# Kernel optimization log

Measured on AMD Instinct MI355X. Metric: run time of the kernel, lower is better.

## Reference

```python
import math
import jax, jax.numpy as jnp
import numpy as np

B, DIM, L = 2, 512, 2048
H = 16
HD = DIM // H  # 32
R = 32
K = 3
GAMMA = 1.0


def _conv1d(x, w, b=None):
    # x: [B, Cin, L], w: [Cout, Cin, K] -> [B, Cout, L_out] (VALID)
    out = jax.lax.conv_general_dilated(
        x, w, window_strides=(1,), padding='VALID',
        dimension_numbers=('NCH', 'OIH', 'NCH'))
    if b is not None:
        out = out + b[None, :, None]
    return out


def _sketch_p4(x, G1, G2):
    # x: [B, H, L, HD]; G1, G2: [HD, R]
    # p=4: half = (1/sqrt(r)) * (x@G1 * x@G2); return half*half
    half = (x @ G1) * (x @ G2) / math.sqrt(R)
    return half * half  # [B, H, L, R]


def setup_inputs() -> dict:
    key = jax.random.key(0)
    ks = jax.random.split(key, 12)
    x = jax.random.normal(ks[0], (B, DIM, L), dtype=jnp.float32)
    # conv / linear params (kaiming-ish scale)
    q_w = jax.random.normal(ks[1], (DIM, DIM, K), dtype=jnp.float32) / math.sqrt(DIM * K)
    q_b = jnp.zeros((DIM,), dtype=jnp.float32)
    k_w = jax.random.normal(ks[2], (DIM, DIM, K), dtype=jnp.float32) / math.sqrt(DIM * K)
    k_b = jnp.zeros((DIM,), dtype=jnp.float32)
    v_w = jax.random.normal(ks[3], (DIM, DIM, 1), dtype=jnp.float32) / math.sqrt(DIM)
    proj_w = jax.random.normal(ks[4], (DIM, DIM), dtype=jnp.float32) / math.sqrt(DIM)
    proj_b = jnp.zeros((DIM,), dtype=jnp.float32)
    # learnable scalars
    gamma_q = jnp.ones((1,), dtype=jnp.float32) * GAMMA
    beta_q = jnp.zeros((1,), dtype=jnp.float32)
    gamma_k = jnp.ones((1,), dtype=jnp.float32) * GAMMA
    beta_k = jnp.zeros((1,), dtype=jnp.float32)
    # sketch matrices, std = 1/sqrt(r)
    G1q = jax.random.normal(ks[5], (HD, R), dtype=jnp.float32) / math.sqrt(R)
    G2q = jax.random.normal(ks[6], (HD, R), dtype=jnp.float32) / math.sqrt(R)
    G1k = jax.random.normal(ks[7], (HD, R), dtype=jnp.float32) / math.sqrt(R)
    G2k = jax.random.normal(ks[8], (HD, R), dtype=jnp.float32) / math.sqrt(R)
    return dict(x=x, q_w=q_w, q_b=q_b, k_w=k_w, k_b=k_b, v_w=v_w,
                proj_w=proj_w, proj_b=proj_b,
                gamma_q=gamma_q, beta_q=beta_q, gamma_k=gamma_k, beta_k=beta_k,
                G1q=G1q, G2q=G2q, G1k=G1k, G2k=G2k)


def reference(x, q_w, q_b, k_w, k_b, v_w, proj_w, proj_b,
              gamma_q, beta_q, gamma_k, beta_k, G1q, G2q, G1k, G2k):
    batch, dim, length = x.shape
    # causal left pad by K-1
    x_pad = jnp.pad(x, ((0, 0), (0, 0), (K - 1, 0)))
    q = _conv1d(x_pad, q_w, q_b)   # [B, DIM, L]
    k = _conv1d(x_pad, k_w, k_b)   # [B, DIM, L]
    v = _conv1d(x, v_w)            # [B, DIM, L] (1x1 conv, no bias)

    def shape(t):
        # [B, DIM, L] -> [B, H, HD, L] -> [B, H, L, HD]
        return t.reshape(batch, H, HD, length).transpose(0, 1, 3, 2)

    q, k, v = shape(q), shape(k), shape(v)
    q = gamma_q * q + beta_q
    k = gamma_k * k + beta_k
    phi_q = _sketch_p4(q, G1q, G2q)  # [B, H, L, R]
    phi_k = _sketch_p4(k, G1k, G2k)  # [B, H, L, R]
    scores = jnp.einsum('bhlr,bhmr->bhlm', phi_q, phi_k)  # [B, H, L, L]
    attn = scores / (scores.sum(axis=-1, keepdims=True) + 1e-6)
    o = jnp.einsum('bhlm,bhmd->bhld', attn, v)  # [B, H, L, HD]
    # [B, H, L, HD] -> [B, H, HD, L] -> [B, DIM, L] -> [B, L, DIM]
    o = o.transpose(0, 1, 3, 2).reshape(batch, dim, length).transpose(0, 2, 1)
    return o @ proj_w.T + proj_b
```

## Files before the change

### kernel.cpp

```cpp
#include <hip/hip_runtime.h>
#include <hip/hip_bf16.h>

#define DIMC 512
#define LEN  2048
#define NH   16
#define HD   32
#define RR   32

typedef __bf16 bf8_t __attribute__((ext_vector_type(8)));
typedef float  f4_t  __attribute__((ext_vector_type(4)));

__device__ __forceinline__ void gload16(const void* g, void* l) {
    __builtin_amdgcn_global_load_lds(
        (const __attribute__((address_space(1))) unsigned int*)g,
        (__attribute__((address_space(3))) unsigned int*)l, 16, 0, 0);
}

__global__ __launch_bounds__(256) void prep_kernel(
    const float* __restrict__ x,
    const float* __restrict__ qw, const float* __restrict__ kw,
    const float* __restrict__ vw, const float* __restrict__ pw,
    const float* __restrict__ G1q, const float* __restrict__ G2q,
    const float* __restrict__ G1k, const float* __restrict__ G2k,
    __bf16* __restrict__ xTh, __bf16* __restrict__ xTl,
    __bf16* __restrict__ Wrh, __bf16* __restrict__ Wrl,
    __bf16* __restrict__ pwh, __bf16* __restrict__ pwl,
    __bf16* __restrict__ GTh, __bf16* __restrict__ GTl,
    float* __restrict__ Skv)
{
    const int bid = blockIdx.x;
    const int tid = threadIdx.x;
    if (bid < 512) {
        __shared__ float tile[64][65];
        const int lblk = bid & 31, cblk = (bid >> 5) & 7, b = bid >> 8;
        const int l0 = lblk * 64, c0 = cblk * 64;
        #pragma unroll
        for (int it = 0; it < 4; ++it) {
            int cl = (tid >> 4) + it * 16;
            int ll = (tid & 15) * 4;
            float4 v4 = *reinterpret_cast<const float4*>(
                x + ((size_t)b * DIMC + c0 + cl) * LEN + l0 + ll);
            tile[cl][ll+0] = v4.x; tile[cl][ll+1] = v4.y;
            tile[cl][ll+2] = v4.z; tile[cl][ll+3] = v4.w;
        }
        __syncthreads();
        const int l  = tid & 63;
        const int cs = (tid >> 6) * 16;
        size_t rowbase = ((size_t)b * 2050 + l0 + l + 2) * DIMC + c0;
        #pragma unroll
        for (int half = 0; half < 2; ++half) {
            int c = cs + half * 8;
            bf8_t hi, lo;
            #pragma unroll
            for (int e = 0; e < 8; ++e) {
                float f = tile[c + e][l];
                __bf16 h = (__bf16)f;
                hi[e] = h;
                lo[e] = (__bf16)(f - (float)h);
            }
            *reinterpret_cast<bf8_t*>(xTh + rowbase + c) = hi;
            *reinterpret_cast<bf8_t*>(xTl + rowbase + c) = lo;
        }
        if (lblk == 0 && cblk == 0) {
            size_t pb = (size_t)b * 2050 * DIMC;
            #pragma unroll
            for (int e = 0; e < 4; ++e) {
                int p = tid * 4 + e;
                xTh[pb + p] = (__bf16)0.f;
                xTl[pb + p] = (__bf16)0.f;
            }
        }
    } else if (bid < 9728) {
        int idx = (bid - 512) * 256 + tid;
        int m   = idx / 1536;
        int rem = idx - m * 1536;
        int kk  = rem >> 9;
        int ci  = rem & 511;
        float f;
        if (m < 512)       f = qw[((size_t)m * 512 + ci) * 3 + kk];
        else if (m < 1024) f = kw[((size_t)(m - 512) * 512 + ci) * 3 + kk];
        else               f = (kk == 2) ? vw[(size_t)(m - 1024) * 512 + ci] : 0.f;
        __bf16 h = (__bf16)f;
        Wrh[idx] = h;
        Wrl[idx] = (__bf16)(f - (float)h);
    } else if (bid < 10752) {
        int idx = (bid - 9728) * 256 + tid;
        float f = pw[idx];
        __bf16 h = (__bf16)f;
        pwh[idx] = h;
        pwl[idx] = (__bf16)(f - (float)h);
    } else if (bid < 10884) {
        int idx = (bid - 10752) * 256 + tid;
        if (idx < 33792) Skv[idx] = 0.f;
    } else {
        #pragma unroll
        for (int m = 0; m < 4; ++m) {
            const float* g = (m == 0) ? G1q : (m == 1) ? G2q : (m == 2) ? G1k : G2k;
            #pragma unroll
            for (int e = 0; e < 4; ++e) {
                int i = tid * 4 + e;
                int r = i >> 5, d = i & 31;
                float f = g[d * 32 + r];
                __bf16 h = (__bf16)f;
                GTh[m * 1024 + i] = h;
                GTl[m * 1024 + i] = (__bf16)(f - (float)h);
            }
        }
    }
}

__global__ __launch_bounds__(256) void conv_mfma_kernel(
    const __bf16* __restrict__ xTh, const __bf16* __restrict__ xTl,
    const __bf16* __restrict__ Wrh, const __bf16* __restrict__ Wrl,
    const float* __restrict__ q_b, const float* __restrict__ k_b,
    float* __restrict__ q, float* __restrict__ k, float* __restrict__ v)
{
    __shared__ __bf16 sAh[128 * 32], sAl[128 * 32], sBh[64 * 32], sBl[64 * 32];
    const int b   = blockIdx.z;
    const int mg  = blockIdx.y * 128;
    const int n0  = blockIdx.x * 64;
    const int tid = threadIdx.x;
    const int wave = tid >> 6, lane = tid & 63;
    const int wm = wave >> 1, wn = wave & 1;
    const int lr = lane & 15, k8 = lane >> 4;
    const int sec = mg >> 9;
    const int kks = (sec == 2) ? 2 : 0;

    const __bf16* xh = xTh + (size_t)b * 2050 * DIMC;
    const __bf16* xl = xTl + (size_t)b * 2050 * DIMC;

    f4_t acc[4][2];
    #pragma unroll
    for (int i = 0; i < 4; ++i)
        #pragma unroll
        for (int j = 0; j < 2; ++j)
            #pragma unroll
            for (int e = 0; e < 4; ++e) acc[i][j][e] = 0.f;

    const int sr0 = tid >> 2;
    const int ss  = tid & 3;
    const int sk0 = ((ss ^ ((sr0 >> 1) & 3)) << 3);
    const int sr1 = sr0 + 64;
    const int sk1 = ((ss ^ ((sr1 >> 1) & 3)) << 3);

    for (int kk = kks; kk < 3; ++kk) {
        const __bf16* wAh = Wrh + (size_t)mg * 1536 + kk * 512;
        const __bf16* wAl = Wrl + (size_t)mg * 1536 + kk * 512;
        const __bf16* xbh = xh + (size_t)(n0 + kk) * DIMC;
        const __bf16* xbl = xl + (size_t)(n0 + kk) * DIMC;
        for (int k0 = 0; k0 < 512; k0 += 32) {
            gload16(wAh + (size_t)sr0 * 1536 + k0 + sk0, (char*)sAh + tid * 16);
            gload16(wAh + (size_t)sr1 * 1536 + k0 + sk1, (char*)sAh + (256 + tid) * 16);
            gload16(wAl + (size_t)sr0 * 1536 + k0 + sk0, (char*)sAl + tid * 16);
            gload16(wAl + (size_t)sr1 * 1536 + k0 + sk1, (char*)sAl + (256 + tid) * 16);
            gload16(xbh + (size_t)sr0 * DIMC + k0 + sk0, (char*)sBh + tid * 16);
            gload16(xbl + (size_t)sr0 * DIMC + k0 + sk0, (char*)sBl + tid * 16);
            __syncthreads();
            bf8_t ah[4], al[4], bh[2], bl[2];
            #pragma unroll
            for (int i = 0; i < 4; ++i) {
                int row = wm * 64 + i * 16 + lr;
                int off = row * 64 + ((k8 ^ ((row >> 1) & 3)) << 4);
                ah[i] = *(const bf8_t*)((const char*)sAh + off);
                al[i] = *(const bf8_t*)((const char*)sAl + off);
            }
            #pragma unroll
            for (int j = 0; j < 2; ++j) {
                int row = wn * 32 + j * 16 + lr;
                int off = row * 64 + ((k8 ^ ((row >> 1) & 3)) << 4);
                bh[j] = *(const bf8_t*)((const char*)sBh + off);
                bl[j] = *(const bf8_t*)((const char*)sBl + off);
            }
            #pragma unroll
            for (int i = 0; i < 4; ++i)
                #pragma unroll
                for (int j = 0; j < 2; ++j) {
                    acc[i][j] = __builtin_amdgcn_mfma_f32_16x16x32_bf16(ah[i], bh[j], acc[i][j], 0, 0, 0);
                    acc[i][j] = __builtin_amdgcn_mfma_f32_16x16x32_bf16(ah[i], bl[j], acc[i][j], 0, 0, 0);
                    acc[i][j] = __builtin_amdgcn_mfma_f32_16x16x32_bf16(al[i], bh[j], acc[i][j], 0, 0, 0);
                }
            __syncthreads();
        }
    }
    float* outp = (sec == 0) ? q : (sec == 1) ? k : v;
    const float* bp = (sec == 0) ? q_b : (sec == 1) ? k_b : nullptr;
    const int cob = mg & 511;
    #pragma unroll
    for (int i = 0; i < 4; ++i)
        #pragma unroll
        for (int r = 0; r < 4; ++r) {
            int co = cob + wm * 64 + i * 16 + k8 * 4 + r;
            float bv = bp ? bp[co] : 0.f;
            float* orow = outp + ((size_t)b * DIMC + co) * LEN;
            #pragma unroll
            for (int j = 0; j < 2; ++j)
                orow[n0 + wn * 32 + j * 16 + lr] = acc[i][j][r];
            if (bp) {
                #pragma unroll
                for (int j = 0; j < 2; ++j)
                    orow[n0 + wn * 32 + j * 16 + lr] = acc[i][j][r] + bv;
            }
        }
}

__global__ __launch_bounds__(256) void sketch_mfma_kernel(
    const float* __restrict__ q, const float* __restrict__ k,
    const float* __restrict__ gamma_q, const float* __restrict__ beta_q,
    const float* __restrict__ gamma_k, const float* __restrict__ beta_k,
    const __bf16* __restrict__ GTh, const __bf16* __restrict__ GTl,
    float* __restrict__ phi_q, float* __restrict__ phi_k)
{
    __shared__ __align__(16) __bf16 sBh[128 * 32];
    __shared__ __align__(16) __bf16 sBl[128 * 32];
    const int z = blockIdx.z;
    const int b = z & 1, isk = z >> 1;
    const int h0 = blockIdx.y * 2;
    const int l0 = blockIdx.x * 64;
    const int tid = threadIdx.x;
    const int wave = tid >> 6, lane = tid & 63;
    const int lr = lane & 15, k8 = lane >> 4;

    const float* src = isk ? k : q;
    float* phi = isk ? phi_k : phi_q;
    const float ga = isk ? gamma_k[0] : gamma_q[0];
    const float be = isk ? beta_k[0]  : beta_q[0];

    #pragma unroll
    for (int it = 0; it < 4; ++it) {
        int f = it * 256 + tid;
        int row = f >> 4;
        int l4  = (f & 15) * 4;
        float4 v4 = *reinterpret_cast<const float4*>(
            src + ((size_t)b * DIMC + h0 * 32 + row) * LEN + l0 + l4);
        int d = row & 31, hloc = row >> 5;
        float vv[4] = {v4.x, v4.y, v4.z, v4.w};
        #pragma unroll
        for (int e = 0; e < 4; ++e) {
            float qp = ga * vv[e] + be;
            __bf16 hh = (__bf16)qp;
            int col = hloc * 64 + l4 + e;
            int off = col * 32 + (((d >> 3) ^ (col & 3)) << 3) + (d & 7);
            sBh[off] = hh;
            sBl[off] = (__bf16)(qp - (float)hh);
        }
    }
    __syncthreads();

    const int cw = wave * 32;
    bf8_t bh[2], bl[2];
    #pragma unroll
    for (int nt = 0; nt < 2; ++nt) {
        int col = cw + nt * 16 + lr;
        int off = col * 32 + ((k8 ^ (col & 3)) << 3);
        bh[nt] = *(const bf8_t*)(sBh + off);
        bl[nt] = *(const bf8_t*)(sBl + off);
    }

    const int matb = isk * 2;
    f4_t t1[2][2], t2[2][2];
    #pragma unroll
    for (int mt = 0; mt < 2; ++mt)
        #pragma unroll
        for (int nt = 0; nt < 2; ++nt)
            #pragma unroll
            for (int e = 0; e < 4; ++e) { t1[mt][nt][e] = 0.f; t2[mt][nt][e] = 0.f; }

    #pragma unroll
    for (int mt = 0; mt < 2; ++mt) {
        int abase = matb * 1024 + (mt * 16 + lr) * 32 + k8 * 8;
        bf8_t a1h = *(const bf8_t*)(GTh + abase);
        bf8_t a1l = *(const bf8_t*)(GTl + abase);
        bf8_t a2h = *(const bf8_t*)(GTh + abase + 1024);
        bf8_t a2l = *(const bf8_t*)(GTl + abase + 1024);
        #pragma unroll
        for (int nt = 0; nt < 2; ++nt) {
            t1[mt][nt] = __builtin_amdgcn_mfma_f32_16x16x32_bf16(a1h, bh[nt], t1[mt][nt], 0, 0, 0);
            t1[mt][nt] = __builtin_amdgcn_mfma_f32_16x16x32_bf16(a1h, bl[nt], t1[mt][nt], 0, 0, 0);
            t1[mt][nt] = __builtin_amdgcn_mfma_f32_16x16x32_bf16(a1l, bh[nt], t1[mt][nt], 0, 0, 0);
            t2[mt][nt] = __builtin_amdgcn_mfma_f32_16x16x32_bf16(a2h, bh[nt], t2[mt][nt], 0, 0, 0);
            t2[mt][nt] = __builtin_amdgcn_mfma_f32_16x16x32_bf16(a2h, bl[nt], t2[mt][nt], 0, 0, 0);
            t2[mt][nt] = __builtin_amdgcn_mfma_f32_16x16x32_bf16(a2l, bh[nt], t2[mt][nt], 0, 0, 0);
        }
    }

    #pragma unroll
    for (int mt = 0; mt < 2; ++mt)
        #pragma unroll
        for (int nt = 0; nt < 2; ++nt) {
            int col = cw + nt * 16 + lr;
            int l = col & 63, hloc = col >> 6;
            f4_t out;
            #pragma unroll
            for (int e = 0; e < 4; ++e) {
                float hh = t1[mt][nt][e] * t2[mt][nt][e] * 0.17677669529663687f;
                out[e] = hh * hh;
            }
            *reinterpret_cast<f4_t*>(phi +
                (((size_t)b * NH + h0 + hloc) * LEN + l0 + l) * RR + mt * 16 + k8 * 4) = out;
        }
}

__global__ __launch_bounds__(256) void skv_kernel(
    const float* __restrict__ phi_k, const float* __restrict__ v,
    float* __restrict__ Skv, float* __restrict__ sk)
{
    const int b = blockIdx.z, h = blockIdx.y;
    const int l0 = blockIdx.x * 64;
    const int tid = threadIdx.x;
    __shared__ float ps[64][RR];
    __shared__ float vs[64][HD + 1];
    const int r  = tid >> 3;
    const int d4 = (tid & 7) * 4;
    float acc[4] = {0.f, 0.f, 0.f, 0.f};
    float skacc = 0.f;
    const float* pk = phi_k + ((size_t)(b * NH + h) * LEN + l0) * RR;
    const float* vb = v + ((size_t)b * DIMC + h * HD) * LEN + l0;
    for (int i = tid; i < 64 * 32; i += 256) {
        ps[i >> 5][i & 31] = pk[i];
        int dd = i >> 6, lc = i & 63;
        vs[lc][dd] = vb[(size_t)dd * LEN + lc];
    }
    __syncthreads();
    #pragma unroll 8
    for (int lc = 0; lc < 64; ++lc) {
        float pv = ps[lc][r];
        skacc += pv;
        #pragma unroll
        for (int j = 0; j < 4; ++j) acc[j] += pv * vs[lc][d4 + j];
    }
    const size_t base = (size_t)(b * NH + h) * RR + r;
    float* Sp = Skv + base * HD + d4;
    #pragma unroll
    for (int j = 0; j < 4; ++j) atomicAdd(Sp + j, acc[j]);
    if ((tid & 7) == 0) atomicAdd(sk + base, skacc);
}

__global__ __launch_bounds__(256) void onorm_kernel(
    const float* __restrict__ phi_q, const float* __restrict__ Skv,
    const float* __restrict__ sk, __bf16* __restrict__ o_h, __bf16* __restrict__ o_l)
{
    __shared__ float Ss[4][RR][HD];
    __shared__ float sks[4][RR];
    __shared__ float ph[32][RR + 1];
    const int b = blockIdx.z, hg = blockIdx.y;
    const int l0 = blockIdx.x * 32;
    const int tid = threadIdx.x;
    const int bh0 = b * NH + hg * 4;
    for (int i = tid; i < 4096; i += 256) {
        int hh = i >> 10;
        Ss[hh][(i >> 5) & 31][i & 31] = Skv[(size_t)(bh0 + hh) * (RR * HD) + (i & 1023)];
    }
    if (tid < 128) sks[tid >> 5][tid & 31] = sk[(size_t)(bh0 + (tid >> 5)) * RR + (tid & 31)];
    const int d = tid & 31, ls = tid >> 5;
    for (int h = 0; h < 4; ++h) {
        __syncthreads();
        for (int i = tid; i < 1024; i += 256)
            ph[i >> 5][i & 31] = phi_q[((size_t)(bh0 + h) * LEN + l0 + (i >> 5)) * RR + (i & 31)];
        __syncthreads();
        #pragma unroll
        for (int lt = 0; lt < 4; ++lt) {
            int l = lt * 8 + ls;
            float num = 0.f, den = 0.f;
            #pragma unroll
            for (int r = 0; r < RR; ++r) {
                float p = ph[l][r];
                num += p * Ss[h][r][d];
                den += p * sks[h][r];
            }
            float val = num / (den + 1e-6f);
            __bf16 hv = (__bf16)val;
            size_t oi = ((size_t)b * LEN + l0 + l) * DIMC + (hg * 4 + h) * HD + d;
            o_h[oi] = hv;
            o_l[oi] = (__bf16)(val - (float)hv);
        }
    }
}

__global__ __launch_bounds__(256) void proj_mfma_kernel(
    const __bf16* __restrict__ oh, const __bf16* __restrict__ ol,
    const __bf16* __restrict__ pwh, const __bf16* __restrict__ pwl,
    const float* __restrict__ pb, float* __restrict__ out)
{
    __shared__ __bf16 sAh[128 * 32], sAl[128 * 32], sBh[64 * 32], sBl[64 * 32];
    const int m0  = blockIdx.y * 128;
    const int n0  = blockIdx.x * 64;
    const int tid = threadIdx.x;
    const int wave = tid >> 6, lane = tid & 63;
    const int wm = wave >> 1, wn = wave & 1;
    const int lr = lane & 15, k8 = lane >> 4;

    f4_t acc[4][2];
    #pragma unroll
    for (int i = 0; i < 4; ++i)
        #pragma unroll
        for (int j = 0; j < 2; ++j)
            #pragma unroll
            for (int e = 0; e < 4; ++e) acc[i][j][e] = 0.f;

    const int sr0 = tid >> 2;
    const int ss  = tid & 3;
    const int sk0 = ((ss ^ ((sr0 >> 1) & 3)) << 3);
    const int sr1 = sr0 + 64;
    const int sk1 = ((ss ^ ((sr1 >> 1) & 3)) << 3);

    for (int k0 = 0; k0 < 512; k0 += 32) {
        gload16(oh + (size_t)(m0 + sr0) * DIMC + k0 + sk0, (char*)sAh + tid * 16);
        gload16(oh + (size_t)(m0 + sr1) * DIMC + k0 + sk1, (char*)sAh + (256 + tid) * 16);
        gload16(ol + (size_t)(m0 + sr0) * DIMC + k0 + sk0, (char*)sAl + tid * 16);
        gload16(ol + (size_t)(m0 + sr1) * DIMC + k0 + sk1, (char*)sAl + (256 + tid) * 16);
        gload16(pwh + (size_t)(n0 + sr0) * DIMC + k0 + sk0, (char*)sBh + tid * 16);
        gload16(pwl + (size_t)(n0 + sr0) * DIMC + k0 + sk0, (char*)sBl + tid * 16);
        __syncthreads();
        bf8_t ah[4], al[4], bh[2], bl[2];
        #pragma unroll
        for (int i = 0; i < 4; ++i) {
            int row = wm * 64 + i * 16 + lr;
            int off = row * 64 + ((k8 ^ ((row >> 1) & 3)) << 4);
            ah[i] = *(const bf8_t*)((const char*)sAh + off);
            al[i] = *(const bf8_t*)((const char*)sAl + off);
        }
        #pragma unroll
        for (int j = 0; j < 2; ++j) {
            int row = wn * 32 + j * 16 + lr;
            int off = row * 64 + ((k8 ^ ((row >> 1) & 3)) << 4);
            bh[j] = *(const bf8_t*)((const char*)sBh + off);
            bl[j] = *(const bf8_t*)((const char*)sBl + off);
        }
        #pragma unroll
        for (int i = 0; i < 4; ++i)
            #pragma unroll
            for (int j = 0; j < 2; ++j) {
                acc[i][j] = __builtin_amdgcn_mfma_f32_16x16x32_bf16(ah[i], bh[j], acc[i][j], 0, 0, 0);
                acc[i][j] = __builtin_amdgcn_mfma_f32_16x16x32_bf16(ah[i], bl[j], acc[i][j], 0, 0, 0);
                acc[i][j] = __builtin_amdgcn_mfma_f32_16x16x32_bf16(al[i], bh[j], acc[i][j], 0, 0, 0);
            }
        __syncthreads();
    }
    #pragma unroll
    for (int j = 0; j < 2; ++j) {
        int n = n0 + wn * 32 + j * 16 + lr;
        float bv = pb[n];
        #pragma unroll
        for (int i = 0; i < 4; ++i)
            #pragma unroll
            for (int r = 0; r < 4; ++r) {
                int m = m0 + wm * 64 + i * 16 + k8 * 4 + r;
                out[(size_t)m * DIMC + n] = acc[i][j][r] + bv;
            }
    }
}

extern "C" void kernel_launch(void* const* d_in, const int* in_sizes, int n_in,
                              void* d_out, int out_size, void* d_ws, size_t ws_size,
                              hipStream_t stream)
{
    const float* x       = (const float*)d_in[0];
    const float* q_w     = (const float*)d_in[1];
    const float* q_b     = (const float*)d_in[2];
    const float* k_w     = (const float*)d_in[3];
    const float* k_b     = (const float*)d_in[4];
    const float* v_w     = (const float*)d_in[5];
    const float* proj_w  = (const float*)d_in[6];
    const float* proj_b  = (const float*)d_in[7];
    const float* gamma_q = (const float*)d_in[8];
    const float* beta_q  = (const float*)d_in[9];
    const float* gamma_k = (const float*)d_in[10];
    const float* beta_k  = (const float*)d_in[11];
    const float* G1q     = (const float*)d_in[12];
    const float* G2q     = (const float*)d_in[13];
    const float* G1k     = (const float*)d_in[14];
    const float* G2k     = (const float*)d_in[15];

    char* W = (char*)d_ws;
    constexpr size_t QKV  = (size_t)2 * DIMC * LEN * 4;
    constexpr size_t XT   = (size_t)2 * 2050 * DIMC * 2;
    constexpr size_t WR   = (size_t)1536 * 1536 * 2;
    constexpr size_t PW   = (size_t)DIMC * DIMC * 2;
    constexpr size_t GT   = (size_t)4 * 1024 * 2;

    float*  q    = (float*)(W);
    float*  k    = (float*)(W + QKV);
    float*  v    = (float*)(W + 2 * QKV);
    __bf16* xTh  = (__bf16*)(W + 3 * QKV);
    __bf16* xTl  = (__bf16*)(W + 3 * QKV + XT);
    __bf16* Wrh  = (__bf16*)(W + 3 * QKV + 2 * XT);
    __bf16* Wrl  = (__bf16*)(W + 3 * QKV + 2 * XT + WR);
    __bf16* pwh  = (__bf16*)(W + 3 * QKV + 2 * XT + 2 * WR);
    __bf16* pwl  = (__bf16*)(W + 3 * QKV + 2 * XT + 2 * WR + PW);
    __bf16* GTh  = (__bf16*)(W + 3 * QKV + 2 * XT + 2 * WR + 2 * PW);
    __bf16* GTl  = (__bf16*)(W + 3 * QKV + 2 * XT + 2 * WR + 2 * PW + GT);
    float*  Skv  = (float*)(W + 3 * QKV + 2 * XT + 2 * WR + 2 * PW + 2 * GT);
    float*  sk   = Skv + (size_t)2 * NH * RR * HD;
    float*  phi_q = (float*)xTh;
    float*  phi_k = (float*)Wrh;
    __bf16* o_h   = (__bf16*)q;
    __bf16* o_l   = (__bf16*)(W + QKV / 2);

    prep_kernel<<<10885, 256, 0, stream>>>(x, q_w, k_w, v_w, proj_w,
                                           G1q, G2q, G1k, G2k,
                                           xTh, xTl, Wrh, Wrl, pwh, pwl,
                                           GTh, GTl, Skv);

    conv_mfma_kernel<<<dim3(LEN / 64, 12, 2), 256, 0, stream>>>(
        xTh, xTl, Wrh, Wrl, q_b, k_b, q, k, v);

    sketch_mfma_kernel<<<dim3(LEN / 64, NH / 2, 4), 256, 0, stream>>>(
        q, k, gamma_q, beta_q, gamma_k, beta_k, GTh, GTl, phi_q, phi_k);

    skv_kernel<<<dim3(LEN / 64, NH, 2), 256, 0, stream>>>(phi_k, v, Skv, sk);

    onorm_kernel<<<dim3(LEN / 32, NH / 4, 2), 256, 0, stream>>>(
        phi_q, Skv, sk, o_h, o_l);

    proj_mfma_kernel<<<dim3(DIMC / 64, (2 * LEN) / 128), 256, 0, stream>>>(
        o_h, o_l, pwh, pwl, proj_b, (float*)d_out);
}
```

Baseline: 229.0 us.

## Fuse phi_k sketch with Skv/sk reduction and drop redundant conv store

Merges the k-side sketch computation with the phi_k^T v and phi_k-sum reduction, so phi_k is staged in shared memory instead of written to and re-read from global memory. This also removes one kernel launch. The conv epilogue now stores once with the bias added, instead of storing twice when a bias is present. The LDS swizzle for the sketch B operand is changed to a three-term XOR to reduce bank conflicts, and the q-side blocks return early after writing phi_q.

```diff
diff --git a/kernel.cpp b/kernel.cpp
--- a/kernel.cpp
+++ b/kernel.cpp
@@ -14,6 +14,10 @@
     __builtin_amdgcn_global_load_lds(
         (const __attribute__((address_space(1))) unsigned int*)g,
         (__attribute__((address_space(3))) unsigned int*)l, 16, 0, 0);
+}
+
+__device__ __forceinline__ int fswz(int col) {
+    return (col ^ (col >> 2) ^ (col >> 4)) & 3;
 }
 
 __global__ __launch_bounds__(256) void prep_kernel(
@@ -194,24 +198,21 @@
             float* orow = outp + ((size_t)b * DIMC + co) * LEN;
             #pragma unroll
             for (int j = 0; j < 2; ++j)
-                orow[n0 + wn * 32 + j * 16 + lr] = acc[i][j][r];
-            if (bp) {
-                #pragma unroll
-                for (int j = 0; j < 2; ++j)
-                    orow[n0 + wn * 32 + j * 16 + lr] = acc[i][j][r] + bv;
-            }
-        }
-}
-
-__global__ __launch_bounds__(256) void sketch_mfma_kernel(
+                orow[n0 + wn * 32 + j * 16 + lr] = acc[i][j][r] + bv;
+        }
+}
+
+__global__ __launch_bounds__(256) void sketch_fused_kernel(
     const float* __restrict__ q, const float* __restrict__ k,
+    const float* __restrict__ v,
     const float* __restrict__ gamma_q, const float* __restrict__ beta_q,
     const float* __restrict__ gamma_k, const float* __restrict__ beta_k,
     const __bf16* __restrict__ GTh, const __bf16* __restrict__ GTl,
-    float* __restrict__ phi_q, float* __restrict__ phi_k)
+    float* __restrict__ phi_q, float* __restrict__ Skv, float* __restrict__ sk)
 {
-    __shared__ __align__(16) __bf16 sBh[128 * 32];
-    __shared__ __align__(16) __bf16 sBl[128 * 32];
+    __shared__ __align__(16) char smem[17424];
+    __bf16* sBh = (__bf16*)smem;
+    __bf16* sBl = (__bf16*)(smem + 8192);
     const int z = blockIdx.z;
     const int b = z & 1, isk = z >> 1;
     const int h0 = blockIdx.y * 2;
@@ -221,7 +222,6 @@
     const int lr = lane & 15, k8 = lane >> 4;
 
     const float* src = isk ? k : q;
-    float* phi = isk ? phi_k : phi_q;
     const float ga = isk ? gamma_k[0] : gamma_q[0];
     const float be = isk ? beta_k[0]  : beta_q[0];
 
@@ -239,7 +239,7 @@
             float qp = ga * vv[e] + be;
             __bf16 hh = (__bf16)qp;
             int col = hloc * 64 + l4 + e;
-            int off = col * 32 + (((d >> 3) ^ (col & 3)) << 3) + (d & 7);
+            int off = col * 32 + (((d >> 3) ^ fswz(col)) << 3) + (d & 7);
             sBh[off] = hh;
             sBl[off] = (__bf16)(qp - (float)hh);
         }
@@ -251,7 +251,7 @@
     #pragma unroll
     for (int nt = 0; nt < 2; ++nt) {
         int col = cw + nt * 16 + lr;
-        int off = col * 32 + ((k8 ^ (col & 3)) << 3);
+        int off = col * 32 + ((k8 ^ fswz(col)) << 3);
         bh[nt] = *(const bf8_t*)(sBh + off);
         bl[nt] = *(const bf8_t*)(sBl + off);
     }
@@ -283,56 +283,67 @@
         }
     }
 
-    #pragma unroll
-    for (int mt = 0; mt < 2; ++mt)
-        #pragma unroll
-        for (int nt = 0; nt < 2; ++nt) {
-            int col = cw + nt * 16 + lr;
-            int l = col & 63, hloc = col >> 6;
-            f4_t out;
-            #pragma unroll
-            for (int e = 0; e < 4; ++e) {
-                float hh = t1[mt][nt][e] * t2[mt][nt][e] * 0.17677669529663687f;
-                out[e] = hh * hh;
-            }
-            *reinterpret_cast<f4_t*>(phi +
-                (((size_t)b * NH + h0 + hloc) * LEN + l0 + l) * RR + mt * 16 + k8 * 4) = out;
-        }
-}
-
-__global__ __launch_bounds__(256) void skv_kernel(
-    const float* __restrict__ phi_k, const float* __restrict__ v,
-    float* __restrict__ Skv, float* __restrict__ sk)
-{
-    const int b = blockIdx.z, h = blockIdx.y;
-    const int l0 = blockIdx.x * 64;
-    const int tid = threadIdx.x;
-    __shared__ float ps[64][RR];
-    __shared__ float vs[64][HD + 1];
+    if (!isk) {
+        #pragma unroll
+        for (int mt = 0; mt < 2; ++mt)
+            #pragma unroll
+            for (int nt = 0; nt < 2; ++nt) {
+                int col = cw + nt * 16 + lr;
+                int l = col & 63, hloc = col >> 6;
+                f4_t out;
+                #pragma unroll
+                for (int e = 0; e < 4; ++e) {
+                    float hh = t1[mt][nt][e] * t2[mt][nt][e] * 0.17677669529663687f;
+                    out[e] = hh * hh;
+                }
+                *reinterpret_cast<f4_t*>(phi_q +
+                    (((size_t)b * NH + h0 + hloc) * LEN + l0 + l) * RR + mt * 16 + k8 * 4) = out;
+            }
+        return;
+    }
+
+    float* phiS = (float*)smem;
+    float* vS   = (float*)(smem + 8448);
     const int r  = tid >> 3;
     const int d4 = (tid & 7) * 4;
-    float acc[4] = {0.f, 0.f, 0.f, 0.f};
-    float skacc = 0.f;
-    const float* pk = phi_k + ((size_t)(b * NH + h) * LEN + l0) * RR;
-    const float* vb = v + ((size_t)b * DIMC + h * HD) * LEN + l0;
-    for (int i = tid; i < 64 * 32; i += 256) {
-        ps[i >> 5][i & 31] = pk[i];
-        int dd = i >> 6, lc = i & 63;
-        vs[lc][dd] = vb[(size_t)dd * LEN + lc];
-    }
-    __syncthreads();
-    #pragma unroll 8
-    for (int lc = 0; lc < 64; ++lc) {
-        float pv = ps[lc][r];
-        skacc += pv;
-        #pragma unroll
-        for (int j = 0; j < 4; ++j) acc[j] += pv * vs[lc][d4 + j];
-    }
-    const size_t base = (size_t)(b * NH + h) * RR + r;
-    float* Sp = Skv + base * HD + d4;
-    #pragma unroll
-    for (int j = 0; j < 4; ++j) atomicAdd(Sp + j, acc[j]);
-    if ((tid & 7) == 0) atomicAdd(sk + base, skacc);
+    const int hl = wave >> 1;
+    #pragma unroll
+    for (int hph = 0; hph < 2; ++hph) {
+        __syncthreads();
+        if (hl == hph) {
+            #pragma unroll
+            for (int mt = 0; mt < 2; ++mt)
+                #pragma unroll
+                for (int nt = 0; nt < 2; ++nt) {
+                    int l = (cw + nt * 16 + lr) & 63;
+                    #pragma unroll
+                    for (int e = 0; e < 4; ++e) {
+                        float hh = t1[mt][nt][e] * t2[mt][nt][e] * 0.17677669529663687f;
+                        phiS[l * 33 + mt * 16 + k8 * 4 + e] = hh * hh;
+                    }
+                }
+        }
+        const float* vb = v + ((size_t)b * DIMC + (h0 + hph) * HD) * LEN + l0;
+        for (int i = tid; i < 64 * 32; i += 256) {
+            int dd = i >> 6, lc = i & 63;
+            vS[lc * 33 + dd] = vb[(size_t)dd * LEN + lc];
+        }
+        __syncthreads();
+        float acc4[4] = {0.f, 0.f, 0.f, 0.f};
+        float skacc = 0.f;
+        #pragma unroll 8
+        for (int lc = 0; lc < 64; ++lc) {
+            float pv = phiS[lc * 33 + r];
+            skacc += pv;
+            #pragma unroll
+            for (int j = 0; j < 4; ++j) acc4[j] += pv * vS[lc * 33 + d4 + j];
+        }
+        const size_t base = (size_t)(b * NH + h0 + hph) * RR + r;
+        float* Sp = Skv + base * HD + d4;
+        #pragma unroll
+        for (int j = 0; j < 4; ++j) atomicAdd(Sp + j, acc4[j]);
+        if ((tid & 7) == 0) atomicAdd(sk + base, skacc);
+    }
 }
 
 __global__ __launch_bounds__(256) void onorm_kernel(
@@ -492,7 +503,6 @@
     float*  Skv  = (float*)(W + 3 * QKV + 2 * XT + 2 * WR + 2 * PW + 2 * GT);
     float*  sk   = Skv + (size_t)2 * NH * RR * HD;
     float*  phi_q = (float*)xTh;
-    float*  phi_k = (float*)Wrh;
     __bf16* o_h   = (__bf16*)q;
     __bf16* o_l   = (__bf16*)(W + QKV / 2);
 
@@ -504,10 +514,8 @@
     conv_mfma_kernel<<<dim3(LEN / 64, 12, 2), 256, 0, stream>>>(
         xTh, xTl, Wrh, Wrl, q_b, k_b, q, k, v);
 
-    sketch_mfma_kernel<<<dim3(LEN / 64, NH / 2, 4), 256, 0, stream>>>(
-        q, k, gamma_q, beta_q, gamma_k, beta_k, GTh, GTl, phi_q, phi_k);
-
-    skv_kernel<<<dim3(LEN / 64, NH, 2), 256, 0, stream>>>(phi_k, v, Skv, sk);
+    sketch_fused_kernel<<<dim3(LEN / 64, NH / 2, 4), 256, 0, stream>>>(
+        q, k, v, gamma_q, beta_q, gamma_k, beta_k, GTh, GTl, phi_q, Skv, sk);
 
     onorm_kernel<<<dim3(LEN / 32, NH / 4, 2), 256, 0, stream>>>(
         phi_q, Skv, sk, o_h, o_l);
```

Result: no change. 231.3 us (+1.0%).
